# Optimization experiments

Hardware: AMD Instinct MI355X
Metric: run time of the kernel (lower is better)

## Reference

```python
import jax, jax.numpy as jnp
import numpy as np

N_NODES = 100000
N_EDGES = 3200000
IN_F = 256
OUT_F = 256


def setup_inputs() -> dict:
    key = jax.random.key(0)
    k_x, k_r, k_c, k_v, k_w = jax.random.split(key, 5)
    x = jax.random.normal(k_x, (N_NODES, IN_F), dtype=jnp.float32)
    edge_rows = jax.random.randint(k_r, (N_EDGES,), 0, N_NODES, dtype=jnp.int32)
    edge_cols = jax.random.randint(k_c, (N_EDGES,), 0, N_NODES, dtype=jnp.int32)
    adj_vals = jax.random.uniform(k_v, (N_EDGES,), dtype=jnp.float32)
    # Xavier-uniform init as in nn.init.xavier_uniform_
    limit = float(np.sqrt(6.0 / (IN_F + OUT_F)))
    weight = jax.random.uniform(k_w, (IN_F, OUT_F), minval=-limit, maxval=limit, dtype=jnp.float32)
    bias = jnp.zeros((OUT_F,), dtype=jnp.float32)
    return {"x": x, "edge_rows": edge_rows, "edge_cols": edge_cols,
            "adj_vals": adj_vals, "weight": weight, "bias": bias}


def reference(x, edge_rows, edge_cols, adj_vals, weight, bias):
    # Dense feature transform + bias: h = x @ W + b  -> [N, OUT_F]
    h = x @ weight + bias
    # Sparse adjacency matmul (SpMM): out[r] = sum_e adj_vals[e] * h[edge_cols[e]]
    msgs = adj_vals[:, None] * h[edge_cols]  # [E, OUT_F]
    out = jax.ops.segment_sum(msgs, edge_rows, num_segments=N_NODES)
    return out
```

## Files before the change

### kernel.cpp

```cpp
#include <hip/hip_runtime.h>

#define N_NODES 100000
#define IN_F 256
#define OUT_F 256
#define NROWS N_NODES
#define NBLK ((NROWS + 255) / 256)
#define MSTRIPS (N_NODES / 32)
#define GEMM_BLOCKS ((MSTRIPS + 3) / 4)

#define RPB 512
#define NBUCKET ((NROWS + RPB - 1) / RPB)
#define E_PER_BLK 4096

typedef float f32x4 __attribute__((ext_vector_type(4)));
typedef __bf16 bf16x8 __attribute__((ext_vector_type(8)));

__global__ __launch_bounds__(256) void prep_w_kernel(const float* __restrict__ W,
                                                     __bf16* __restrict__ Wt) {
    int n = blockIdx.x;
    int k = threadIdx.x;
    Wt[n * IN_F + k] = (__bf16)W[k * OUT_F + n];
}

__global__ __launch_bounds__(256, 2) void gemm_count_kernel(const float* __restrict__ x,
                                                            const __bf16* __restrict__ Wt,
                                                            const float* __restrict__ bias,
                                                            __bf16* __restrict__ h,
                                                            const int* __restrict__ rows,
                                                            int* __restrict__ deg, int nE) {
    if (blockIdx.x >= GEMM_BLOCKS) {
        int i = (blockIdx.x - GEMM_BLOCKS) * 1024 + threadIdx.x * 4;
        if (i + 3 < nE) {
            int4 rr = *(const int4*)(rows + i);
            atomicAdd(&deg[rr.x], 1);
            atomicAdd(&deg[rr.y], 1);
            atomicAdd(&deg[rr.z], 1);
            atomicAdd(&deg[rr.w], 1);
        } else {
            for (int e = i; e < nE; ++e) atomicAdd(&deg[rows[e]], 1);
        }
        return;
    }

    int wave = (blockIdx.x << 2) | (threadIdx.x >> 6);
    if (wave >= MSTRIPS) return;
    int lane = threadIdx.x & 63;
    int r16 = lane & 15;
    int quad = lane >> 4;

    const float*  xp0 = x + (size_t)(wave * 32 + r16) * IN_F + quad * 8;
    const float*  xp1 = xp0 + (size_t)16 * IN_F;
    const __bf16* wp  = Wt + (size_t)r16 * IN_F + quad * 8;

    f32x4 acc[2][16];
#pragma unroll
    for (int m = 0; m < 2; ++m)
#pragma unroll
        for (int i = 0; i < 16; ++i) acc[m][i] = (f32x4){0.f, 0.f, 0.f, 0.f};

#pragma unroll
    for (int k0 = 0; k0 < IN_F; k0 += 32) {
        f32x4 x00 = *(const f32x4*)(xp0 + k0);
        f32x4 x01 = *(const f32x4*)(xp0 + k0 + 4);
        f32x4 x10 = *(const f32x4*)(xp1 + k0);
        f32x4 x11 = *(const f32x4*)(xp1 + k0 + 4);
        bf16x8 a0, a1;
#pragma unroll
        for (int j = 0; j < 4; ++j) {
            a0[j] = (__bf16)x00[j]; a0[j + 4] = (__bf16)x01[j];
            a1[j] = (__bf16)x10[j]; a1[j + 4] = (__bf16)x11[j];
        }
#pragma unroll
        for (int nt = 0; nt < 16; ++nt) {
            bf16x8 b = *(const bf16x8*)(wp + (size_t)nt * 16 * IN_F + k0);
            acc[0][nt] = __builtin_amdgcn_mfma_f32_16x16x32_bf16(a0, b, acc[0][nt], 0, 0, 0);
            acc[1][nt] = __builtin_amdgcn_mfma_f32_16x16x32_bf16(a1, b, acc[1][nt], 0, 0, 0);
        }
    }

#pragma unroll
    for (int m = 0; m < 2; ++m)
#pragma unroll
        for (int nt = 0; nt < 16; ++nt) {
            float bv = bias[nt * 16 + r16];
            __bf16* hp = h + (size_t)(wave * 32 + m * 16 + quad * 4) * OUT_F + nt * 16 + r16;
#pragma unroll
            for (int r = 0; r < 4; ++r)
                hp[(size_t)r * OUT_F] = (__bf16)(acc[m][nt][r] + bv);
        }
}

__global__ __launch_bounds__(256) void partial_kernel(const int* __restrict__ deg,
                                                      int* __restrict__ partial) {
    __shared__ int s[256];
    int i = blockIdx.x * 256 + threadIdx.x;
    s[threadIdx.x] = (i < NROWS) ? deg[i] : 0;
    __syncthreads();
    for (int d = 128; d > 0; d >>= 1) {
        if (threadIdx.x < d) s[threadIdx.x] += s[threadIdx.x + d];
        __syncthreads();
    }
    if (threadIdx.x == 0) partial[blockIdx.x] = s[0];
}

__global__ __launch_bounds__(512) void scan_partial_kernel(const int* __restrict__ partial,
                                                           int* __restrict__ blockoff,
                                                           int* __restrict__ row_start, int nE) {
    __shared__ int s[512];
    int t = threadIdx.x;
    int v = (t < NBLK) ? partial[t] : 0;
    s[t] = v;
    __syncthreads();
    for (int d = 1; d < 512; d <<= 1) {
        int u = (t >= d) ? s[t - d] : 0;
        __syncthreads();
        s[t] += u;
        __syncthreads();
    }
    if (t < NBLK) blockoff[t] = s[t] - v;
    if (t == 0) row_start[NROWS] = nE;
}

__global__ __launch_bounds__(256) void scan_rows_kernel(const int* __restrict__ deg,
                                                        const int* __restrict__ blockoff,
                                                        int* __restrict__ row_start) {
    __shared__ int s[256];
    int t = threadIdx.x;
    int i = blockIdx.x * 256 + t;
    int v = (i < NROWS) ? deg[i] : 0;
    s[t] = v;
    __syncthreads();
    for (int d = 1; d < 256; d <<= 1) {
        int u = (t >= d) ? s[t - d] : 0;
        __syncthreads();
        s[t] += u;
        __syncthreads();
    }
    if (i < NROWS) row_start[i] = blockoff[blockIdx.x] + s[t] - v;
}

__global__ __launch_bounds__(256) void init_bucket_kernel(const int* __restrict__ row_start,
                                                          int* __restrict__ bucket_cur) {
    int t = threadIdx.x;
    if (t < NBUCKET) {
        int gr = t * RPB;
        bucket_cur[t] = row_start[gr < NROWS ? gr : NROWS];
    }
}

__global__ __launch_bounds__(256) void bin_kernel(const int* __restrict__ rows,
                                                  const int* __restrict__ cols,
                                                  const float* __restrict__ vals,
                                                  int* __restrict__ bucket_cur,
                                                  unsigned long long* __restrict__ inter,
                                                  int nE) {
    __shared__ int cnt[NBUCKET];
    __shared__ int off[NBUCKET];
    int t = threadIdx.x;
    for (int i = t; i < NBUCKET; i += 256) cnt[i] = 0;
    __syncthreads();
    int base = blockIdx.x * E_PER_BLK;
#pragma unroll
    for (int j = 0; j < 16; ++j) {
        int e = base + j * 256 + t;
        if (e < nE) atomicAdd(&cnt[rows[e] >> 9], 1);
    }
    __syncthreads();
    for (int i = t; i < NBUCKET; i += 256)
        off[i] = cnt[i] ? atomicAdd(&bucket_cur[i], cnt[i]) : 0;
    __syncthreads();
#pragma unroll
    for (int j = 0; j < 16; ++j) {
        int e = base + j * 256 + t;
        if (e < nE) {
            int r = rows[e];
            unsigned c = (unsigned)cols[e];
            unsigned vb = __float_as_uint(vals[e]);
            int b = r >> 9;
            int p = atomicAdd(&off[b], 1);
            inter[p] = ((unsigned long long)vb << 32) |
                       ((unsigned long long)((unsigned)(r & (RPB - 1)) << 17)) | c;
        }
    }
}

__global__ __launch_bounds__(256) void bucket_sort_kernel(const int* __restrict__ row_start,
                                                          const unsigned long long* __restrict__ inter,
                                                          long long* __restrict__ sorted) {
    __shared__ int cur[RPB];
    int t = threadIdx.x;
    int r0 = blockIdx.x * RPB;
    for (int i = t; i < RPB; i += 256) {
        int gr = r0 + i;
        cur[i] = row_start[gr < NROWS ? gr : NROWS];
    }
    __syncthreads();
    int eb = row_start[r0];
    int gend = r0 + RPB; if (gend > NROWS) gend = NROWS;
    int ee = row_start[gend];
    for (int e = eb + t; e < ee; e += 256) {
        unsigned long long pk = inter[e];
        unsigned meta = (unsigned)pk;
        int lr = (meta >> 17) & (RPB - 1);
        unsigned c = meta & 0x1FFFFu;
        int pos = atomicAdd(&cur[lr], 1);
        sorted[pos] = (long long)((pk & 0xFFFFFFFF00000000ull) | c);
    }
}

__global__ __launch_bounds__(256, 4) void spmm_csr_kernel(const int* __restrict__ row_start,
                                                          const long long* __restrict__ sorted,
                                                          const __bf16* __restrict__ h,
                                                          float* __restrict__ out) {
    int half = threadIdx.x >> 5;
    int sub  = threadIdx.x & 31;
    int r = blockIdx.x * 8 + half;
    int e0 = row_start[r];
    int e1 = row_start[r + 1];

    f32x4 a0 = {0.f,0.f,0.f,0.f}, a1 = {0.f,0.f,0.f,0.f};
    f32x4 b0 = {0.f,0.f,0.f,0.f}, b1 = {0.f,0.f,0.f,0.f};

    int e = e0;
    if (e + 8 <= e1) {
        long long p[8];
#pragma unroll
        for (int j = 0; j < 8; ++j) p[j] = __builtin_nontemporal_load(sorted + e + j);
        e += 8;
        for (; e + 8 <= e1; e += 8) {
            bf16x8 g[8];
#pragma unroll
            for (int j = 0; j < 8; ++j)
                g[j] = ((const bf16x8*)(h + (size_t)(int)p[j] * OUT_F))[sub];
            long long q[8];
#pragma unroll
            for (int j = 0; j < 8; ++j) q[j] = __builtin_nontemporal_load(sorted + e + j);
#pragma unroll
            for (int j = 0; j < 8; ++j) {
                float v = __int_as_float((int)(p[j] >> 32));
#pragma unroll
                for (int k = 0; k < 4; ++k) {
                    if (j & 1) { b0[k] += v * (float)g[j][k]; b1[k] += v * (float)g[j][k + 4]; }
                    else       { a0[k] += v * (float)g[j][k]; a1[k] += v * (float)g[j][k + 4]; }
                }
            }
#pragma unroll
            for (int j = 0; j < 8; ++j) p[j] = q[j];
        }
        {
            bf16x8 g[8];
#pragma unroll
            for (int j = 0; j < 8; ++j)
                g[j] = ((const bf16x8*)(h + (size_t)(int)p[j] * OUT_F))[sub];
#pragma unroll
            for (int j = 0; j < 8; ++j) {
                float v = __int_as_float((int)(p[j] >> 32));
#pragma unroll
                for (int k = 0; k < 4; ++k) {
                    if (j & 1) { b0[k] += v * (float)g[j][k]; b1[k] += v * (float)g[j][k + 4]; }
                    else       { a0[k] += v * (float)g[j][k]; a1[k] += v * (float)g[j][k + 4]; }
                }
            }
        }
    }
    if (e < e1) {
        int rem = e1 - e;
        long long t[8];
#pragma unroll
        for (int j = 0; j < 8; ++j) {
            int idx = e + j;
            if (idx > e1 - 1) idx = e1 - 1;
            t[j] = __builtin_nontemporal_load(sorted + idx);
        }
        bf16x8 g[8];
#pragma unroll
        for (int j = 0; j < 8; ++j)
            g[j] = ((const bf16x8*)(h + (size_t)(int)t[j] * OUT_F))[sub];
#pragma unroll
        for (int j = 0; j < 8; ++j) {
            float v = (j < rem) ? __int_as_float((int)(t[j] >> 32)) : 0.f;
#pragma unroll
            for (int k = 0; k < 4; ++k) {
                if (j & 1) { b0[k] += v * (float)g[j][k]; b1[k] += v * (float)g[j][k + 4]; }
                else       { a0[k] += v * (float)g[j][k]; a1[k] += v * (float)g[j][k + 4]; }
            }
        }
    }
#pragma unroll
    for (int k = 0; k < 4; ++k) { a0[k] += b0[k]; a1[k] += b1[k]; }
    float* op = out + (size_t)r * OUT_F + sub * 8;
    ((f32x4*)op)[0] = a0;
    ((f32x4*)op)[1] = a1;
}

extern "C" void kernel_launch(void* const* d_in, const int* in_sizes, int n_in,
                              void* d_out, int out_size, void* d_ws, size_t ws_size,
                              hipStream_t stream) {
    const float* x         = (const float*)d_in[0];
    const int*   edge_rows = (const int*)d_in[1];
    const int*   edge_cols = (const int*)d_in[2];
    const float* adj_vals  = (const float*)d_in[3];
    const float* weight    = (const float*)d_in[4];
    const float* bias      = (const float*)d_in[5];
    float* out = (float*)d_out;
    int nE = in_sizes[1];

    char* w = (char*)d_ws;
    __bf16* h  = (__bf16*)w;  w += (size_t)N_NODES * OUT_F * sizeof(__bf16);
    __bf16* Wt = (__bf16*)w;  w += (size_t)IN_F * OUT_F * sizeof(__bf16);
    int* deg       = (int*)w; w += (size_t)NROWS * 4;
    int* row_start = (int*)w; w += (size_t)(NROWS + 1) * 4 + 12;
    int* partial   = (int*)w; w += (size_t)NBLK * 4;
    int* blockoff  = (int*)w; w += (size_t)NBLK * 4 + 8;
    int* bucket_cur = (int*)w; w += (size_t)NBUCKET * 4 + 16;
    long long* sorted = (long long*)w;

    unsigned long long* inter = (unsigned long long*)d_out;

    hipMemsetAsync(deg, 0, (size_t)NROWS * sizeof(int), stream);
    prep_w_kernel<<<OUT_F, IN_F, 0, stream>>>(weight, Wt);

    int countBlocks = (nE + 1023) / 1024;
    gemm_count_kernel<<<GEMM_BLOCKS + countBlocks, 256, 0, stream>>>(x, Wt, bias, h,
                                                                     edge_rows, deg, nE);

    partial_kernel<<<NBLK, 256, 0, stream>>>(deg, partial);
    scan_partial_kernel<<<1, 512, 0, stream>>>(partial, blockoff, row_start, nE);
    scan_rows_kernel<<<NBLK, 256, 0, stream>>>(deg, blockoff, row_start);
    init_bucket_kernel<<<1, 256, 0, stream>>>(row_start, bucket_cur);

    int binBlocks = (nE + E_PER_BLK - 1) / E_PER_BLK;
    bin_kernel<<<binBlocks, 256, 0, stream>>>(edge_rows, edge_cols, adj_vals,
                                              bucket_cur, inter, nE);
    bucket_sort_kernel<<<NBUCKET, 256, 0, stream>>>(row_start, inter, sorted);

    spmm_csr_kernel<<<NROWS / 8, 256, 0, stream>>>(row_start, sorted, h, out);
}
```

Before: 696.7 us.

## Fuse edge binning into GEMM kernel using fixed-capacity buckets with overflow list

Binning of edges into row buckets now runs inside the GEMM launch, replacing the separate degree-count pass. Each bucket gets a fixed 16K-slot region instead of offsets taken from the prefix scan, so binning no longer waits for the scan; edges beyond capacity go to an overflow index list that the bucket sort pass re-reads. Bucket size drops to 256 rows, and the GEMM is split into two column-half waves per strip to raise wave count and cut accumulator registers. The cost is per-thread row caching, an overflow path whose correctness depends on the overflow count staying within its cap, and every bucket-sort block scanning the whole overflow list.

```diff
diff --git a/kernel.cpp b/kernel.cpp
--- a/kernel.cpp
+++ b/kernel.cpp
@@ -6,11 +6,16 @@
 #define NROWS N_NODES
 #define NBLK ((NROWS + 255) / 256)
 #define MSTRIPS (N_NODES / 32)
-#define GEMM_BLOCKS ((MSTRIPS + 3) / 4)
-
-#define RPB 512
+
+#define GWAVES (MSTRIPS * 2)
+#define GEMM_BLOCKS ((GWAVES + 3) / 4)
+
+#define RPB 256
 #define NBUCKET ((NROWS + RPB - 1) / RPB)
+#define CAP 16384
+#define CAPSH 14
 #define E_PER_BLK 4096
+#define MAX_OV 8192
 
 typedef float f32x4 __attribute__((ext_vector_type(4)));
 typedef __bf16 bf16x8 __attribute__((ext_vector_type(8)));
@@ -22,41 +27,122 @@
     Wt[n * IN_F + k] = (__bf16)W[k * OUT_F + n];
 }
 
-__global__ __launch_bounds__(256, 2) void gemm_count_kernel(const float* __restrict__ x,
-                                                            const __bf16* __restrict__ Wt,
-                                                            const float* __restrict__ bias,
-                                                            __bf16* __restrict__ h,
-                                                            const int* __restrict__ rows,
-                                                            int* __restrict__ deg, int nE) {
+__global__ __launch_bounds__(256, 2) void gemm_bin_kernel(const float* __restrict__ x,
+                                                          const __bf16* __restrict__ Wt,
+                                                          const float* __restrict__ bias,
+                                                          __bf16* __restrict__ h,
+                                                          const int* __restrict__ rows,
+                                                          const int* __restrict__ cols,
+                                                          const float* __restrict__ vals,
+                                                          int* __restrict__ deg,
+                                                          int* __restrict__ bcnt,
+                                                          int* __restrict__ ov_cnt,
+                                                          int* __restrict__ ov_idx,
+                                                          unsigned long long* __restrict__ inter,
+                                                          int nE) {
+    __shared__ int cnt[NBUCKET];
+    __shared__ int off[NBUCKET];
+
     if (blockIdx.x >= GEMM_BLOCKS) {
-        int i = (blockIdx.x - GEMM_BLOCKS) * 1024 + threadIdx.x * 4;
-        if (i + 3 < nE) {
-            int4 rr = *(const int4*)(rows + i);
-            atomicAdd(&deg[rr.x], 1);
-            atomicAdd(&deg[rr.y], 1);
-            atomicAdd(&deg[rr.z], 1);
-            atomicAdd(&deg[rr.w], 1);
-        } else {
-            for (int e = i; e < nE; ++e) atomicAdd(&deg[rows[e]], 1);
+        int bblk = blockIdx.x - GEMM_BLOCKS;
+        int t = threadIdx.x;
+        for (int i = t; i < NBUCKET; i += 256) cnt[i] = 0;
+        __syncthreads();
+        int base = bblk * E_PER_BLK;
+        int r_[16];
+#pragma unroll
+        for (int j = 0; j < 4; ++j) {
+            int e = base + (j * 256 + t) * 4;
+            if (e + 3 < nE) {
+                int4 rr = *(const int4*)(rows + e);
+                r_[j * 4 + 0] = rr.x; r_[j * 4 + 1] = rr.y;
+                r_[j * 4 + 2] = rr.z; r_[j * 4 + 3] = rr.w;
+                atomicAdd(&cnt[rr.x >> 8], 1); atomicAdd(&deg[rr.x], 1);
+                atomicAdd(&cnt[rr.y >> 8], 1); atomicAdd(&deg[rr.y], 1);
+                atomicAdd(&cnt[rr.z >> 8], 1); atomicAdd(&deg[rr.z], 1);
+                atomicAdd(&cnt[rr.w >> 8], 1); atomicAdd(&deg[rr.w], 1);
+            } else {
+#pragma unroll
+                for (int k = 0; k < 4; ++k) {
+                    int ee = e + k;
+                    if (ee < nE) {
+                        int r = rows[ee];
+                        r_[j * 4 + k] = r;
+                        atomicAdd(&cnt[r >> 8], 1);
+                        atomicAdd(&deg[r], 1);
+                    } else r_[j * 4 + k] = -1;
+                }
+            }
+        }
+        __syncthreads();
+        for (int i = t; i < NBUCKET; i += 256) {
+            int c = cnt[i];
+            off[i] = c ? ((i << CAPSH) + atomicAdd(&bcnt[i], c)) : 0;
+        }
+        __syncthreads();
+#pragma unroll
+        for (int j = 0; j < 4; ++j) {
+            int e = base + (j * 256 + t) * 4;
+            if (e + 3 < nE) {
+                int4 cc = *(const int4*)(cols + e);
+                float4 vv = *(const float4*)(vals + e);
+                int rr[4] = {r_[j*4+0], r_[j*4+1], r_[j*4+2], r_[j*4+3]};
+                int cc4[4] = {cc.x, cc.y, cc.z, cc.w};
+                float vv4[4] = {vv.x, vv.y, vv.z, vv.w};
+#pragma unroll
+                for (int k = 0; k < 4; ++k) {
+                    int r = rr[k];
+                    int b = r >> 8;
+                    int p = atomicAdd(&off[b], 1);
+                    unsigned long long pk =
+                        ((unsigned long long)__float_as_uint(vv4[k]) << 32) |
+                        ((unsigned)(r & (RPB - 1)) << 17) | (unsigned)cc4[k];
+                    if (p < ((b + 1) << CAPSH)) inter[p] = pk;
+                    else {
+                        int o = atomicAdd(ov_cnt, 1);
+                        if (o < MAX_OV) ov_idx[o] = e + k;
+                    }
+                }
+            } else {
+#pragma unroll
+                for (int k = 0; k < 4; ++k) {
+                    int ee = e + k;
+                    int r = r_[j * 4 + k];
+                    if (r >= 0) {
+                        int b = r >> 8;
+                        int p = atomicAdd(&off[b], 1);
+                        unsigned long long pk =
+                            ((unsigned long long)__float_as_uint(vals[ee]) << 32) |
+                            ((unsigned)(r & (RPB - 1)) << 17) | (unsigned)cols[ee];
+                        if (p < ((b + 1) << CAPSH)) inter[p] = pk;
+                        else {
+                            int o = atomicAdd(ov_cnt, 1);
+                            if (o < MAX_OV) ov_idx[o] = ee;
+                        }
+                    }
+                }
+            }
         }
         return;
     }
 
     int wave = (blockIdx.x << 2) | (threadIdx.x >> 6);
-    if (wave >= MSTRIPS) return;
+    if (wave >= GWAVES) return;
+    int strip = wave >> 1;
+    int nh = wave & 1;
     int lane = threadIdx.x & 63;
     int r16 = lane & 15;
     int quad = lane >> 4;
 
-    const float*  xp0 = x + (size_t)(wave * 32 + r16) * IN_F + quad * 8;
+    const float*  xp0 = x + (size_t)(strip * 32 + r16) * IN_F + quad * 8;
     const float*  xp1 = xp0 + (size_t)16 * IN_F;
-    const __bf16* wp  = Wt + (size_t)r16 * IN_F + quad * 8;
-
-    f32x4 acc[2][16];
+    const __bf16* wp  = Wt + (size_t)(nh * 128 + r16) * IN_F + quad * 8;
+
+    f32x4 acc[2][8];
 #pragma unroll
     for (int m = 0; m < 2; ++m)
 #pragma unroll
-        for (int i = 0; i < 16; ++i) acc[m][i] = (f32x4){0.f, 0.f, 0.f, 0.f};
+        for (int i = 0; i < 8; ++i) acc[m][i] = (f32x4){0.f, 0.f, 0.f, 0.f};
 
 #pragma unroll
     for (int k0 = 0; k0 < IN_F; k0 += 32) {
@@ -71,7 +157,7 @@
             a1[j] = (__bf16)x10[j]; a1[j + 4] = (__bf16)x11[j];
         }
 #pragma unroll
-        for (int nt = 0; nt < 16; ++nt) {
+        for (int nt = 0; nt < 8; ++nt) {
             bf16x8 b = *(const bf16x8*)(wp + (size_t)nt * 16 * IN_F + k0);
             acc[0][nt] = __builtin_amdgcn_mfma_f32_16x16x32_bf16(a0, b, acc[0][nt], 0, 0, 0);
             acc[1][nt] = __builtin_amdgcn_mfma_f32_16x16x32_bf16(a1, b, acc[1][nt], 0, 0, 0);
@@ -81,9 +167,10 @@
 #pragma unroll
     for (int m = 0; m < 2; ++m)
 #pragma unroll
-        for (int nt = 0; nt < 16; ++nt) {
-            float bv = bias[nt * 16 + r16];
-            __bf16* hp = h + (size_t)(wave * 32 + m * 16 + quad * 4) * OUT_F + nt * 16 + r16;
+        for (int nt = 0; nt < 8; ++nt) {
+            int col = nh * 128 + nt * 16 + r16;
+            float bv = bias[col];
+            __bf16* hp = h + (size_t)(strip * 32 + m * 16 + quad * 4) * OUT_F + col;
 #pragma unroll
             for (int r = 0; r < 4; ++r)
                 hp[(size_t)r * OUT_F] = (__bf16)(acc[m][nt][r] + bv);
@@ -139,72 +226,55 @@
     if (i < NROWS) row_start[i] = blockoff[blockIdx.x] + s[t] - v;
 }
 
-__global__ __launch_bounds__(256) void init_bucket_kernel(const int* __restrict__ row_start,
-                                                          int* __restrict__ bucket_cur) {
-    int t = threadIdx.x;
-    if (t < NBUCKET) {
-        int gr = t * RPB;
-        bucket_cur[t] = row_start[gr < NROWS ? gr : NROWS];
-    }
-}
-
-__global__ __launch_bounds__(256) void bin_kernel(const int* __restrict__ rows,
-                                                  const int* __restrict__ cols,
-                                                  const float* __restrict__ vals,
-                                                  int* __restrict__ bucket_cur,
-                                                  unsigned long long* __restrict__ inter,
-                                                  int nE) {
-    __shared__ int cnt[NBUCKET];
-    __shared__ int off[NBUCKET];
-    int t = threadIdx.x;
-    for (int i = t; i < NBUCKET; i += 256) cnt[i] = 0;
-    __syncthreads();
-    int base = blockIdx.x * E_PER_BLK;
-#pragma unroll
-    for (int j = 0; j < 16; ++j) {
-        int e = base + j * 256 + t;
-        if (e < nE) atomicAdd(&cnt[rows[e] >> 9], 1);
-    }
-    __syncthreads();
-    for (int i = t; i < NBUCKET; i += 256)
-        off[i] = cnt[i] ? atomicAdd(&bucket_cur[i], cnt[i]) : 0;
-    __syncthreads();
-#pragma unroll
-    for (int j = 0; j < 16; ++j) {
-        int e = base + j * 256 + t;
-        if (e < nE) {
-            int r = rows[e];
-            unsigned c = (unsigned)cols[e];
-            unsigned vb = __float_as_uint(vals[e]);
-            int b = r >> 9;
-            int p = atomicAdd(&off[b], 1);
-            inter[p] = ((unsigned long long)vb << 32) |
-                       ((unsigned long long)((unsigned)(r & (RPB - 1)) << 17)) | c;
-        }
-    }
-}
-
 __global__ __launch_bounds__(256) void bucket_sort_kernel(const int* __restrict__ row_start,
                                                           const unsigned long long* __restrict__ inter,
+                                                          const int* __restrict__ bcnt,
+                                                          const int* __restrict__ ov_cnt,
+                                                          const int* __restrict__ ov_idx,
+                                                          const int* __restrict__ rows,
+                                                          const int* __restrict__ cols,
+                                                          const float* __restrict__ vals,
                                                           long long* __restrict__ sorted) {
     __shared__ int cur[RPB];
     int t = threadIdx.x;
-    int r0 = blockIdx.x * RPB;
-    for (int i = t; i < RPB; i += 256) {
-        int gr = r0 + i;
-        cur[i] = row_start[gr < NROWS ? gr : NROWS];
+    int b = blockIdx.x;
+    int r0 = b << 8;
+    {
+        int gr = r0 + t;
+        cur[t] = row_start[gr < NROWS ? gr : NROWS];
     }
     __syncthreads();
-    int eb = row_start[r0];
-    int gend = r0 + RPB; if (gend > NROWS) gend = NROWS;
-    int ee = row_start[gend];
-    for (int e = eb + t; e < ee; e += 256) {
-        unsigned long long pk = inter[e];
+    int n = bcnt[b]; if (n > CAP) n = CAP;
+    const unsigned long long* src = inter + ((size_t)b << CAPSH);
+    int base2 = 0;
+    for (; base2 + 1024 <= n; base2 += 1024) {
+        unsigned long long pk[4];
+#pragma unroll
+        for (int j = 0; j < 4; ++j) pk[j] = src[base2 + j * 256 + t];
+#pragma unroll
+        for (int j = 0; j < 4; ++j) {
+            unsigned meta = (unsigned)pk[j];
+            int lr = (meta >> 17) & (RPB - 1);
+            int pos = atomicAdd(&cur[lr], 1);
+            sorted[pos] = (long long)((pk[j] & 0xFFFFFFFF00000000ull) | (meta & 0x1FFFFu));
+        }
+    }
+    for (int e = base2 + t; e < n; e += 256) {
+        unsigned long long pk = src[e];
         unsigned meta = (unsigned)pk;
         int lr = (meta >> 17) & (RPB - 1);
-        unsigned c = meta & 0x1FFFFu;
         int pos = atomicAdd(&cur[lr], 1);
-        sorted[pos] = (long long)((pk & 0xFFFFFFFF00000000ull) | c);
+        sorted[pos] = (long long)((pk & 0xFFFFFFFF00000000ull) | (meta & 0x1FFFFu));
+    }
+    int m = *ov_cnt; if (m > MAX_OV) m = MAX_OV;
+    for (int i = t; i < m; i += 256) {
+        int e = ov_idx[i];
+        int r = rows[e];
+        if ((r >> 8) == b) {
+            int pos = atomicAdd(&cur[r & (RPB - 1)], 1);
+            sorted[pos] = (long long)(((unsigned long long)__float_as_uint(vals[e]) << 32) |
+                                      (unsigned)cols[e]);
+        }
     }
 }
 
@@ -305,34 +375,37 @@
     float* out = (float*)d_out;
     int nE = in_sizes[1];
 
+    #define ALIGN64(p) (char*)(((size_t)(p) + 63) & ~(size_t)63)
     char* w = (char*)d_ws;
-    __bf16* h  = (__bf16*)w;  w += (size_t)N_NODES * OUT_F * sizeof(__bf16);
-    __bf16* Wt = (__bf16*)w;  w += (size_t)IN_F * OUT_F * sizeof(__bf16);
-    int* deg       = (int*)w; w += (size_t)NROWS * 4;
-    int* row_start = (int*)w; w += (size_t)(NROWS + 1) * 4 + 12;
-    int* partial   = (int*)w; w += (size_t)NBLK * 4;
-    int* blockoff  = (int*)w; w += (size_t)NBLK * 4 + 8;
-    int* bucket_cur = (int*)w; w += (size_t)NBUCKET * 4 + 16;
+    __bf16* h  = (__bf16*)w;  w = ALIGN64(w + (size_t)N_NODES * OUT_F * sizeof(__bf16));
+    __bf16* Wt = (__bf16*)w;  w = ALIGN64(w + (size_t)IN_F * OUT_F * sizeof(__bf16));
+    int* deg    = (int*)w;    w += (size_t)NROWS * 4;
+    int* bcnt   = (int*)w;    w += (size_t)NBUCKET * 4;
+    int* ov_cnt = (int*)w;    w = ALIGN64(w + 16);
+    int* ov_idx = (int*)w;    w = ALIGN64(w + (size_t)MAX_OV * 4);
+    int* row_start = (int*)w; w = ALIGN64(w + (size_t)(NROWS + 1) * 4);
+    int* partial   = (int*)w; w = ALIGN64(w + (size_t)NBLK * 4);
+    int* blockoff  = (int*)w; w = ALIGN64(w + (size_t)NBLK * 4);
     long long* sorted = (long long*)w;
 
     unsigned long long* inter = (unsigned long long*)d_out;
 
-    hipMemsetAsync(deg, 0, (size_t)NROWS * sizeof(int), stream);
+    hipMemsetAsync(deg, 0, (size_t)((char*)ov_cnt - (char*)deg) + 16, stream);
     prep_w_kernel<<<OUT_F, IN_F, 0, stream>>>(weight, Wt);
 
-    int countBlocks = (nE + 1023) / 1024;
-    gemm_count_kernel<<<GEMM_BLOCKS + countBlocks, 256, 0, stream>>>(x, Wt, bias, h,
-                                                                     edge_rows, deg, nE);
+    int binBlocks = (nE + E_PER_BLK - 1) / E_PER_BLK;
+    gemm_bin_kernel<<<GEMM_BLOCKS + binBlocks, 256, 0, stream>>>(
+        x, Wt, bias, h, edge_rows, edge_cols, adj_vals,
+        deg, bcnt, ov_cnt, ov_idx, inter, nE);
 
     partial_kernel<<<NBLK, 256, 0, stream>>>(deg, partial);
     scan_partial_kernel<<<1, 512, 0, stream>>>(partial, blockoff, row_start, nE);
     scan_rows_kernel<<<NBLK, 256, 0, stream>>>(deg, blockoff, row_start);
-    init_bucket_kernel<<<1, 256, 0, stream>>>(row_start, bucket_cur);
-
-    int binBlocks = (nE + E_PER_BLK - 1) / E_PER_BLK;
-    bin_kernel<<<binBlocks, 256, 0, stream>>>(edge_rows, edge_cols, adj_vals,
-                                              bucket_cur, inter, nE);
-    bucket_sort_kernel<<<NBUCKET, 256, 0, stream>>>(row_start, inter, sorted);
+
+    bucket_sort_kernel<<<NBUCKET, 256, 0, stream>>>(row_start, inter, bcnt,
+                                                    ov_cnt, ov_idx,
+                                                    edge_rows, edge_cols, adj_vals,
+                                                    sorted);
 
     spmm_csr_kernel<<<NROWS / 8, 256, 0, stream>>>(row_start, sorted, h, out);
 }
```

Result: faster. 677.3 us (-2.8%).
